# Kernel optimization log

Measured on AMD Instinct MI355X. Metric: run time of the kernel, lower is better.

## Reference

```python
import jax, jax.numpy as jnp
import numpy as np

ALPHA, GAMMA = 0.25, 2.0
MD_THRES = 0.5
BF, AF, VAR = 1.0, 0.5, 1.0  # mining_param chosen to exercise the DAS (dynamic anchor selection) path
BETA = 1.0 / 9.0
EPS = 1e-8


def rbox_corners(boxes):
    # boxes [N,5] = (cx, cy, w, h, angle_deg) -> corners [N,4,2]
    cx, cy, w, h, a = (boxes[:, i] for i in range(5))
    t = a * (jnp.pi / 180.0)
    c, s = jnp.cos(t), jnp.sin(t)
    lx = jnp.array([-0.5, 0.5, 0.5, -0.5], boxes.dtype)
    ly = jnp.array([-0.5, -0.5, 0.5, 0.5], boxes.dtype)
    dx = w[:, None] * lx[None, :]
    dy = h[:, None] * ly[None, :]
    x = cx[:, None] + dx * c[:, None] - dy * s[:, None]
    y = cy[:, None] + dx * s[:, None] + dy * c[:, None]
    return jnp.stack([x, y], axis=-1)


def _pts_in_poly(pts, poly):
    # pts [P,2], poly [4,2] convex quad -> [P] bool
    e = jnp.roll(poly, -1, axis=0) - poly
    rel = pts[:, None, :] - poly[None, :, :]
    cr = e[None, :, 0] * rel[:, :, 1] - e[None, :, 1] * rel[:, :, 0]
    return jnp.all(cr >= -1e-6, axis=1) | jnp.all(cr <= 1e-6, axis=1)


def _pair_inter_area(ca, cb):
    # exact convex quad-quad intersection area; ca, cb: [4,2]
    p, q = ca, cb
    r = jnp.roll(ca, -1, axis=0) - ca
    s = jnp.roll(cb, -1, axis=0) - cb
    rxs = r[:, None, 0] * s[None, :, 1] - r[:, None, 1] * s[None, :, 0]  # [4,4]
    qp = q[None, :, :] - p[:, None, :]
    qpxs = qp[..., 0] * s[None, :, 1] - qp[..., 1] * s[None, :, 0]
    qpxr = qp[..., 0] * r[:, None, 1] - qp[..., 1] * r[:, None, 0]
    denom = jnp.where(jnp.abs(rxs) > 1e-10, rxs, 1.0)
    t = qpxs / denom
    u = qpxr / denom
    valid = (jnp.abs(rxs) > 1e-10) & (t >= 0) & (t <= 1) & (u >= 0) & (u <= 1)
    ipts = p[:, None, :] + t[..., None] * r[:, None, :]  # [4,4,2]
    cand = jnp.concatenate([ca, cb, ipts.reshape(16, 2)], axis=0)  # [24,2]
    mask = jnp.concatenate([_pts_in_poly(ca, cb), _pts_in_poly(cb, ca), valid.reshape(16)])
    n = mask.sum()
    center = (cand * mask[:, None]).sum(0) / jnp.maximum(n, 1)
    d = cand - center
    ang = jnp.where(mask, jnp.arctan2(d[:, 1], d[:, 0]), 1e9)
    order = jnp.argsort(ang)  # valid points first, CCW order
    sp = cand[order]
    sm = mask[order]
    sp = jnp.where(sm[:, None], sp, sp[0])  # pad with first vertex (zero shoelace contribution)
    nx = jnp.roll(sp, -1, axis=0)
    area = 0.5 * jnp.abs(jnp.sum(sp[:, 0] * nx[:, 1] - nx[:, 0] * sp[:, 1]))
    return jnp.where(n >= 3, area, 0.0)


def rbox_iou(boxes_a, boxes_b, indicator, thresh=0.1):
    # exact rotated IoU, computed only where axis-aligned indicator >= thresh (else 0)
    ca = rbox_corners(boxes_a)
    cb = rbox_corners(boxes_b)
    inter = jax.vmap(lambda a: jax.vmap(lambda b: _pair_inter_area(a, b))(cb))(ca)  # [N,M]
    area_a = (boxes_a[:, 2] * boxes_a[:, 3])[:, None]
    area_b = (boxes_b[:, 2] * boxes_b[:, 3])[None, :]
    iou = inter / (area_a + area_b - inter + EPS)
    return jnp.where(indicator >= thresh, iou, 0.0)


def min_area_square(rb):
    s = jnp.maximum(rb[:, 2], rb[:, 3]) * 0.5
    return jnp.stack([rb[:, 0] - s, rb[:, 1] - s, rb[:, 0] + s, rb[:, 1] + s], axis=1)


def bbox_overlaps(a, b):
    # axis-aligned IoU, a [N,4], b [M,4] (xyxy)
    lt = jnp.maximum(a[:, None, :2], b[None, :, :2])
    rb = jnp.minimum(a[:, None, 2:], b[None, :, 2:])
    wh = jnp.clip(rb - lt, 0.0)
    inter = wh[..., 0] * wh[..., 1]
    aa = (a[:, 2] - a[:, 0]) * (a[:, 3] - a[:, 1])
    ab = (b[:, 2] - b[:, 0]) * (b[:, 3] - b[:, 1])
    return inter / (aa[:, None] + ab[None, :] - inter + EPS)


def box_encode(ex, gt):
    gw = jnp.maximum(gt[:, 2], 1.0)
    gh = jnp.maximum(gt[:, 3], 1.0)
    dx = (gt[:, 0] - ex[:, 0]) / ex[:, 2]
    dy = (gt[:, 1] - ex[:, 1]) / ex[:, 3]
    dw = jnp.log(gw / ex[:, 2])
    dh = jnp.log(gh / ex[:, 3])
    dt = jnp.tan(gt[:, 4] * jnp.pi / 180.0) - jnp.tan(ex[:, 4] * jnp.pi / 180.0)
    return jnp.stack([dx, dy, dw, dh, dt], axis=1)


def _image_loss(cls, reg, anc, ranc, ann):
    A, C = cls.shape
    M = ann.shape[0]
    gt = ann[:, :5]
    labels = ann[:, 5].astype(jnp.int32)
    cls = jnp.clip(cls, 1e-4, 1.0 - 1e-4)
    ov_bf = rbox_iou(anc, gt, bbox_overlaps(min_area_square(anc), min_area_square(gt)))
    ov_af = rbox_iou(ranc, gt, bbox_overlaps(min_area_square(ranc), min_area_square(gt)))
    md = jnp.abs(BF * ov_bf + AF * ov_af - jnp.abs(ov_af - ov_bf) ** VAR)
    md = jax.lax.stop_gradient(md)  # original computes overlaps via numpy (no grad)
    iou_max = md.max(1)
    iou_argmax = md.argmax(1)
    pos = iou_max >= MD_THRES
    max_gt = md.max(0)
    argmax_gt = md.argmax(0)
    force = jnp.zeros((A,), jnp.int32).at[argmax_gt].add((max_gt < MD_THRES).astype(jnp.int32)) > 0
    pos = pos | force
    num_pos = pos.sum()
    # DAS matching weights (rows only meaningful at positive anchors; computed full + masked)
    md_p = jnp.where(pos[:, None], md, -jnp.inf)
    max_pos = md_p.max(0)   # [M]
    arg_pos = md_p.argmax(0)
    pos_mask = (md >= MD_THRES) & pos[:, None]
    pos_mask = pos_mask.at[arg_pos, jnp.arange(M)].set(True)
    comp = jnp.where(pos_mask, 1.0 - max_pos[None, :], md)
    mw_max = (comp + md).max(1)  # matching_weight.max(1)[0]
    # classification targets: -1 ignore / 0 neg / 1 pos-class
    assigned = gt[iou_argmax]
    alab = labels[iou_argmax]
    onehot = alab[:, None] == jnp.arange(C)[None, :]
    tgt = jnp.broadcast_to(jnp.where(iou_max < MD_THRES - 0.1, 0.0, -1.0)[:, None], (A, C))
    tgt = jnp.where(pos[:, None], 0.0, tgt)
    tgt = jnp.where(pos[:, None] & onehot, 1.0, tgt)
    af = jnp.where(tgt == 1.0, ALPHA, 1.0 - ALPHA)
    fw = af * jnp.where(tgt == 1.0, 1.0 - cls, cls) ** GAMMA
    bce = -(tgt * jnp.log(cls + 1e-6) + (1.0 - tgt) * jnp.log(1.0 - cls + 1e-6))
    sw = jnp.where(tgt == 0.0, 1.0, 0.0)
    sw = jnp.where(pos[:, None] & onehot, mw_max[:, None] + 1.0, sw)
    cls_loss = jnp.where(tgt != -1.0, fw * bce * sw, 0.0)
    cls_l = cls_loss.sum() / jnp.maximum(num_pos.astype(cls.dtype), 1.0)
    reg_t = box_encode(anc, assigned)
    diff = jnp.abs(reg - reg_t)
    sl1 = jnp.where(diff < BETA, 0.5 * diff ** 2 / BETA, diff - 0.5 * BETA) * mw_max[:, None]
    sl1 = jnp.where(pos[:, None], sl1, 0.0)
    reg_l = jnp.where(num_pos > 0, sl1.sum() / jnp.maximum(num_pos * 5, 1).astype(cls.dtype), 0.0)
    return cls_l, reg_l


def _forward(classifications, regressions, anchors, refined_achors, annotations):
    B = classifications.shape[0]
    cl, rl = [], []
    for j in range(B):  # small fixed batch loop, as in the original
        c, r = _image_loss(classifications[j], regressions[j], anchors[j], refined_achors[j], annotations[j])
        cl.append(c)
        rl.append(r)
    loss_cls = jnp.stack(cl).mean(keepdims=True)
    loss_reg = jnp.stack(rl).mean(keepdims=True)
    return loss_cls, loss_reg


def _rand_boxes(key, shape):
    k1, k2, k3, k4, k5 = jax.random.split(key, 5)
    cx = jax.random.uniform(k1, shape, minval=32.0, maxval=992.0)
    cy = jax.random.uniform(k2, shape, minval=32.0, maxval=992.0)
    w = jax.random.uniform(k3, shape, minval=16.0, maxval=160.0)
    h = jax.random.uniform(k4, shape, minval=16.0, maxval=160.0)
    a = jax.random.uniform(k5, shape, minval=-30.0, maxval=30.0)
    return jnp.stack([cx, cy, w, h, a], axis=-1)


def setup_inputs() -> dict:
    key = jax.random.key(0)
    ks = jax.random.split(key, 6)
    B, A, M, C = 2, 16384, 32, 15
    classifications = jax.random.uniform(ks[0], (B, A, C), minval=0.02, maxval=0.98)
    regressions = 0.1 * jax.random.normal(ks[1], (B, A, 5))
    anchors = _rand_boxes(ks[2], (B, A))
    noise = 0.05 * jax.random.normal(ks[3], (B, A, 5))
    refined_achors = anchors + noise * jnp.array([8.0, 8.0, 4.0, 4.0, 5.0])
    gt = _rand_boxes(ks[4], (B, M))
    labels = jax.random.randint(ks[5], (B, M, 1), 0, C).astype(jnp.float32)
    annotations = jnp.concatenate([gt, labels], axis=-1)  # all labels valid (!= -1)
    return {"classifications": classifications, "regressions": regressions, "anchors": anchors,
            "refined_achors": refined_achors, "annotations": annotations}


def reference(classifications, regressions, anchors, refined_achors, annotations):
    return _forward(classifications, regressions, anchors, refined_achors, annotations)
```

## Files before the change

### kernel.cpp

```cpp
#include <hip/hip_runtime.h>
#include <math.h>

typedef unsigned long long u64;
typedef unsigned int u32;

static constexpr int A = 16384;
static constexpr int M = 32;
static constexpr int C = 15;
static constexpr int B = 2;
static constexpr int NBLK = A / 32;
static constexpr int NBUCKET = 64;
static constexpr int SEGCAP  = 4096;
static constexpr int CAP = NBUCKET * SEGCAP;

static constexpr double PI_D = 3.14159265358979323846;

static constexpr size_t OFF_MD      = 0;
static constexpr size_t OFF_LIST    = OFF_MD + (size_t)B*A*M*4;
static constexpr size_t OFF_PALL    = OFF_LIST + (size_t)CAP*4;
static constexpr size_t OFF_PPOS    = OFF_PALL + (size_t)B*M*NBLK*8;
static constexpr size_t OFF_PCNT    = OFF_PPOS + (size_t)B*M*NBLK*8;
static constexpr size_t OFF_KEYALL  = OFF_PCNT + (size_t)B*NBLK*4;
static constexpr size_t OFF_KEYPOS  = OFF_KEYALL + (size_t)B*M*8;
static constexpr size_t OFF_IOUMAX  = OFF_KEYPOS + (size_t)B*M*8;
static constexpr size_t OFF_IOUARG  = OFF_IOUMAX + (size_t)B*A*4;
static constexpr size_t OFF_POS     = OFF_IOUARG + (size_t)B*A*4;
static constexpr size_t OFF_MAXPOS  = OFF_POS + (size_t)B*A*4;
static constexpr size_t OFF_ARGPOS  = OFF_MAXPOS + (size_t)B*M*4;
static constexpr size_t OFF_NPBASE  = OFF_ARGPOS + (size_t)B*M*4;
static constexpr size_t OFF_NUMPOS  = OFF_NPBASE + (size_t)B*4;
static constexpr size_t OFF_SUMS    = (OFF_NUMPOS + (size_t)B*4 + 7) & ~(size_t)7;
static constexpr size_t OFF_CNTS    = OFF_SUMS + 4*8;
static constexpr size_t CNTS_BYTES  = (size_t)NBUCKET * 32 * 4;

__device__ inline double aa_square_iou(double cx1, double cy1, double s1,
                                       double cx2, double cy2, double s2) {
    double lx = fmax(cx1 - s1, cx2 - s2), ly = fmax(cy1 - s1, cy2 - s2);
    double rx = fmin(cx1 + s1, cx2 + s2), ry = fmin(cy1 + s1, cy2 + s2);
    double w = fmax(rx - lx, 0.0), h = fmax(ry - ly, 0.0);
    double inter = w * h;
    double aa = (2.0 * s1) * (2.0 * s1);
    double ab = (2.0 * s2) * (2.0 * s2);
    return inter / (aa + ab - inter + 1e-8);
}

__device__ inline void rbox_corners1(double cx, double cy, double w, double h,
                                     double adeg, double* X, double* Y) {
    double t = adeg * (PI_D / 180.0);
    double c = cos(t), s = sin(t);
    const double lx[4] = {-0.5, 0.5, 0.5, -0.5};
    const double ly[4] = {-0.5, -0.5, 0.5, 0.5};
#pragma unroll
    for (int i = 0; i < 4; ++i) {
        double dx = w * lx[i], dy = h * ly[i];
        X[i] = cx + dx * c - dy * s;
        Y[i] = cy + dx * s + dy * c;
    }
}

__device__ inline double edges_in_quad_cross_sum(const double* PX, const double* PY,
                                                 const double* QX, const double* QY) {
    double s = 0.0;
#pragma unroll
    for (int k = 0; k < 4; ++k) {
        double x0 = PX[k], y0 = PY[k];
        double x1 = PX[(k + 1) & 3], y1 = PY[(k + 1) & 3];
        double ex = x1 - x0, ey = y1 - y0;
        double t0 = 0.0, t1 = 1.0;
        bool empty = false;
#pragma unroll
        for (int e = 0; e < 4; ++e) {
            double qx0 = QX[e], qy0 = QY[e];
            double qex = QX[(e + 1) & 3] - qx0;
            double qey = QY[(e + 1) & 3] - qy0;
            double d0 = qex * (y0 - qy0) - qey * (x0 - qx0);
            double d1 = qex * (y1 - qy0) - qey * (x1 - qx0);
            if (d0 < 0.0 && d1 < 0.0) empty = true;
            else if (d0 < 0.0) t0 = fmax(t0, d0 / (d0 - d1));
            else if (d1 < 0.0) t1 = fmin(t1, d0 / (d0 - d1));
        }
        if (!empty && t1 > t0) {
            double ax = x0 + t0 * ex, ay = y0 + t0 * ey;
            double bx = x0 + t1 * ex, by = y0 + t1 * ey;
            s += ax * by - ay * bx;
        }
    }
    return s;
}

__device__ inline double quad_inter_area(const double* AX, const double* AY,
                                         const double* BX, const double* BY) {
    double s = edges_in_quad_cross_sum(AX, AY, BX, BY) +
               edges_in_quad_cross_sum(BX, BY, AX, AY);
    return 0.5 * fabs(s);
}

__device__ inline u64 pack_key(float v, u32 inv_idx) {
    return ((u64)__float_as_uint(v) << 32) | (u64)inv_idx;
}

__global__ void k_gate(const float* __restrict__ anc, const float* __restrict__ ranc,
                       const float* __restrict__ ann, float* __restrict__ md,
                       u32* __restrict__ list, u32* __restrict__ cnts,
                       double* __restrict__ sums) {
    __shared__ u32 l_cnt, l_base;
    __shared__ u32 l_idx[256];
    int tid = threadIdx.x;
    if (tid == 0) l_cnt = 0;
    __syncthreads();

    int t = blockIdx.x * 256 + tid;
    if (t < 4) sums[t] = 0.0;
    int m = t & (M - 1);
    int a = (t >> 5) & (A - 1);
    int b = t >> 19;

    const float* pa = anc + ((size_t)(b * A + a)) * 5;
    const float* pr = ranc + ((size_t)(b * A + a)) * 5;
    const float* pg = ann + ((size_t)(b * M + m)) * 6;

    double cxg = pg[0], cyg = pg[1];
    double sg = 0.5 * fmax((double)pg[2], (double)pg[3]);
    double i_bf = aa_square_iou(pa[0], pa[1], 0.5 * fmax((double)pa[2], (double)pa[3]),
                                cxg, cyg, sg);
    double i_af = aa_square_iou(pr[0], pr[1], 0.5 * fmax((double)pr[2], (double)pr[3]),
                                cxg, cyg, sg);
    bool g = (i_bf >= 0.1) || (i_af >= 0.1);
    md[t] = 0.0f;

    if (g) {
        u32 s = atomicAdd(&l_cnt, 1u);
        l_idx[s] = (u32)t;
    }
    __syncthreads();
    u32 n = l_cnt;
    int bucket = blockIdx.x & (NBUCKET - 1);
    if (tid == 0 && n) l_base = atomicAdd(&cnts[bucket * 32], n);
    __syncthreads();
    if ((u32)tid < n) {
        u32 slot = l_base + (u32)tid;
        if (slot < SEGCAP) list[bucket * SEGCAP + slot] = l_idx[tid];
    }
}

__global__ void k_geom(const float* __restrict__ anc, const float* __restrict__ ranc,
                       const float* __restrict__ ann, const u32* __restrict__ list,
                       const u32* __restrict__ cnts, float* __restrict__ md) {
    for (u32 i = blockIdx.x * 256 + threadIdx.x; i < (u32)CAP; i += gridDim.x * 256) {
        u32 bucket = i & (NBUCKET - 1);
        u32 slot = i >> 6;
        if (slot >= cnts[bucket * 32]) continue;
        u32 t = list[bucket * SEGCAP + slot];
        int m = t & (M - 1);
        int a = (t >> 5) & (A - 1);
        int b = t >> 19;
        const float* pa = anc + ((size_t)(b * A + a)) * 5;
        const float* pr = ranc + ((size_t)(b * A + a)) * 5;
        const float* pg = ann + ((size_t)(b * M + m)) * 6;

        double cxg = pg[0], cyg = pg[1], wg = pg[2], hg = pg[3], ag = pg[4];
        double sg = 0.5 * fmax(wg, hg);
        double cxa = pa[0], cya = pa[1], wa = pa[2], ha = pa[3], aa = pa[4];
        double cxr = pr[0], cyr = pr[1], wr = pr[2], hr = pr[3], ar = pr[4];

        double i_bf = aa_square_iou(cxa, cya, 0.5 * fmax(wa, ha), cxg, cyg, sg);
        double i_af = aa_square_iou(cxr, cyr, 0.5 * fmax(wr, hr), cxg, cyg, sg);

        double GX[4], GY[4];
        rbox_corners1(cxg, cyg, wg, hg, ag, GX, GY);
        double areaG = wg * hg;
        double ov_bf = 0.0, ov_af = 0.0;
        if (i_bf >= 0.1) {
            double X[4], Y[4];
            rbox_corners1(cxa, cya, wa, ha, aa, X, Y);
            double inter = quad_inter_area(X, Y, GX, GY);
            ov_bf = inter / (wa * ha + areaG - inter + 1e-8);
        }
        if (i_af >= 0.1) {
            double X[4], Y[4];
            rbox_corners1(cxr, cyr, wr, hr, ar, X, Y);
            double inter = quad_inter_area(X, Y, GX, GY);
            ov_af = inter / (wr * hr + areaG - inter + 1e-8);
        }
        md[t] = (float)fabs(ov_bf + 0.5 * ov_af - fabs(ov_af - ov_bf));
    }
}

__global__ void k_rowcol(const float* __restrict__ md, u64* __restrict__ pAll,
                         u64* __restrict__ pPos, u32* __restrict__ pCnt,
                         float* __restrict__ iou_max, int* __restrict__ iou_arg,
                         int* __restrict__ pos) {
    int blk = blockIdx.x, b = blockIdx.y, tid = threadIdx.x;
    int a0 = blk * 32;
    const float4* src = (const float4*)(md + (size_t)(b * A + a0) * M);
    float4 v4 = src[tid];
    int rr = tid >> 3, c0 = (tid & 7) * 4;
    float vv[4] = {v4.x, v4.y, v4.z, v4.w};

    u64 rowk = 0;
#pragma unroll
    for (int j = 0; j < 4; ++j) {
        u64 k = pack_key(vv[j], 0xFFFFFFFFu - (u32)(c0 + j));
        if (k > rowk) rowk = k;
    }
#pragma unroll
    for (int off = 1; off < 8; off <<= 1) {
        u64 o = __shfl_xor(rowk, off, 8);
        if (o > rowk) rowk = o;
    }
    float rmax = __uint_as_float((u32)(rowk >> 32));
    int p = (rmax >= 0.5f) ? 1 : 0;

    __shared__ u64 lAll[32][32];
    __shared__ u64 lPos[32][32];
    __shared__ int lcnt[32];
    u32 inva = 0xFFFFFFFFu - (u32)(a0 + rr);
#pragma unroll
    for (int j = 0; j < 4; ++j) {
        u64 ck = pack_key(vv[j], inva);
        lAll[rr][c0 + j] = ck;
        lPos[rr][c0 + j] = p ? ck : 0ull;
    }
    if ((tid & 7) == 0) {
        int idx = b * A + a0 + rr;
        iou_max[idx] = rmax;
        iou_arg[idx] = (int)(0xFFFFFFFFu - (u32)(rowk & 0xFFFFFFFFull));
        pos[idx] = p;
        lcnt[rr] = p;
    }
    __syncthreads();
    if (tid < 32) {
        u64 ka = 0, kp = 0;
#pragma unroll
        for (int r = 0; r < 32; ++r) {
            u64 x = lAll[r][tid]; if (x > ka) ka = x;
            u64 y = lPos[r][tid]; if (y > kp) kp = y;
        }
        pAll[((size_t)(b * M + tid)) * NBLK + blk] = ka;
        pPos[((size_t)(b * M + tid)) * NBLK + blk] = kp;
        if (tid == 0) {
            int c = 0;
#pragma unroll
            for (int r = 0; r < 32; ++r) c += lcnt[r];
            pCnt[b * NBLK + blk] = (u32)c;
        }
    }
}

__global__ void k_cols(const u64* __restrict__ pAll, const u64* __restrict__ pPos,
                       const u32* __restrict__ pCnt, u64* __restrict__ keyAll,
                       u64* __restrict__ keyPos, int* __restrict__ npbase) {
    int m = blockIdx.x, b = blockIdx.y, tid = threadIdx.x;
    const u64* pa = pAll + ((size_t)(b * M + m)) * NBLK;
    const u64* pp = pPos + ((size_t)(b * M + m)) * NBLK;
    u64 ka = pa[tid], kp = pp[tid];
    u64 ka2 = pa[tid + 256], kp2 = pp[tid + 256];
    if (ka2 > ka) ka = ka2;
    if (kp2 > kp) kp = kp2;
    __shared__ u64 sa[256], sp[256];
    sa[tid] = ka; sp[tid] = kp;
    __syncthreads();
    for (int s = 128; s > 0; s >>= 1) {
        if (tid < s) {
            if (sa[tid + s] > sa[tid]) sa[tid] = sa[tid + s];
            if (sp[tid + s] > sp[tid]) sp[tid] = sp[tid + s];
        }
        __syncthreads();
    }
    if (tid == 0) {
        keyAll[b * M + m] = sa[0];
        keyPos[b * M + m] = sp[0];
    }
    if (m == 0) {
        __shared__ int sc[256];
        sc[tid] = (int)(pCnt[b * NBLK + tid] + pCnt[b * NBLK + tid + 256]);
        __syncthreads();
        for (int s = 128; s > 0; s >>= 1) {
            if (tid < s) sc[tid] += sc[tid + s];
            __syncthreads();
        }
        if (tid == 0) npbase[b] = sc[0];
    }
}

__global__ void k_fix(const u64* __restrict__ keyAll, const u64* __restrict__ keyPos,
                      const float* __restrict__ md, const int* __restrict__ npbase,
                      int* __restrict__ pos, float* __restrict__ max_pos,
                      int* __restrict__ arg_pos, int* __restrict__ num_pos) {
    int b = blockIdx.x, tid = threadIdx.x;
    __shared__ int s_list[32];
    __shared__ int s_nf, s_new;
    if (tid == 0) { s_nf = 0; s_new = 0; }
    __syncthreads();
    if (tid < 32) {
        u64 k = keyAll[b * M + tid];
        float mx = __uint_as_float((u32)(k >> 32));
        if (mx < 0.5f) {
            int fa = (int)(0xFFFFFFFFu - (u32)(k & 0xFFFFFFFFull));
            int slot = atomicAdd(&s_nf, 1);
            s_list[slot] = fa;
        }
    }
    __syncthreads();
    if (tid < s_nf) {
        int fa = s_list[tid];
        int old = atomicOr(&pos[b * A + fa], 1);
        if (old == 0) atomicAdd(&s_new, 1);
    }
    __syncthreads();
    if (tid < 32) {
        u64 best = keyPos[b * M + tid];
        int nf = s_nf;
        for (int f = 0; f < nf; ++f) {
            int fa = s_list[f];
            float v = md[((size_t)(b * A + fa)) * M + tid];
            u64 k = pack_key(v, 0xFFFFFFFFu - (u32)fa);
            if (k > best) best = k;
        }
        int idx = b * M + tid;
        if (best == 0ull) {
            max_pos[idx] = 0.0f;
            arg_pos[idx] = -1;
        } else {
            max_pos[idx] = __uint_as_float((u32)(best >> 32));
            arg_pos[idx] = (int)(0xFFFFFFFFu - (u32)(best & 0xFFFFFFFFull));
        }
    }
    if (tid == 0) num_pos[b] = npbase[b] + s_new;
}

__global__ void k_loss(const float* __restrict__ cls_in, const float* __restrict__ reg_in,
                       const float* __restrict__ anc, const float* __restrict__ ann,
                       const float* __restrict__ md,
                       const float* __restrict__ iou_max, const int* __restrict__ iou_arg,
                       const int* __restrict__ pos,
                       const float* __restrict__ max_pos, const int* __restrict__ arg_pos,
                       double* __restrict__ sums) {
    int b = blockIdx.y;
    int tid = threadIdx.x;
    int a = blockIdx.x * 256 + tid;

    __shared__ float s_maxpos[M];
    __shared__ int s_argpos[M];
    if (tid < M) {
        s_maxpos[tid] = max_pos[b * M + tid];
        s_argpos[tid] = arg_pos[b * M + tid];
    }
    __syncthreads();

    double csum = 0.0, rsum = 0.0;
    if (a < A) {
        int t = b * A + a;
        float imax = iou_max[t];
        int iarg = iou_arg[t];
        int p = pos[t];

        const float* row = md + (size_t)t * M;
        float mwf = -INFINITY;
#pragma unroll
        for (int m = 0; m < M; ++m) {
            float v = row[m];
            bool pm = (p && v >= 0.5f) || (a == s_argpos[m]);
            float val = pm ? (1.0f - s_maxpos[m] + v) : (v + v);
            mwf = fmaxf(mwf, val);
        }
        double mw = (double)mwf;

        const float* g = ann + ((size_t)(b * M + iarg)) * 6;
        int lab = (int)g[5];
        const float* cp = cls_in + (size_t)t * C;
#pragma unroll
        for (int c = 0; c < C; ++c) {
            double x = (double)cp[c];
            x = fmin(fmax(x, 1e-4), 1.0 - 1e-4);
            double tgt;
            if (p) tgt = (c == lab) ? 1.0 : 0.0;
            else   tgt = (imax < 0.4f) ? 0.0 : -1.0;
            if (tgt >= 0.0) {
                bool one = (tgt == 1.0);
                double af = one ? 0.25 : 0.75;
                double q = one ? (1.0 - x) : x;
                double fw = af * q * q;
                double bce = one ? -log(x + 1e-6) : -log(1.0 - x + 1e-6);
                double sw = one ? (mw + 1.0) : 1.0;
                csum += fw * bce * sw;
            }
        }
        if (p) {
            const float* pa = anc + (size_t)t * 5;
            double gw = fmax((double)g[2], 1.0);
            double gh = fmax((double)g[3], 1.0);
            double rt0 = ((double)g[0] - (double)pa[0]) / (double)pa[2];
            double rt1 = ((double)g[1] - (double)pa[1]) / (double)pa[3];
            double rt2 = log(gw / (double)pa[2]);
            double rt3 = log(gh / (double)pa[3]);
            double rt4 = tan((double)g[4] * (PI_D / 180.0)) - tan((double)pa[4] * (PI_D / 180.0));
            double rt[5] = {rt0, rt1, rt2, rt3, rt4};
            const float* rg = reg_in + (size_t)t * 5;
#pragma unroll
            for (int k = 0; k < 5; ++k) {
                double d = fabs((double)rg[k] - rt[k]);
                double s = (d < (1.0 / 9.0)) ? (0.5 * d * d * 9.0) : (d - 0.5 / 9.0);
                rsum += s * mw;
            }
        }
    }
    __shared__ double scs[256];
    __shared__ double srs[256];
    scs[tid] = csum;
    srs[tid] = rsum;
    __syncthreads();
    for (int s = 128; s > 0; s >>= 1) {
        if (tid < s) { scs[tid] += scs[tid + s]; srs[tid] += srs[tid + s]; }
        __syncthreads();
    }
    if (tid == 0) {
        atomicAdd(&sums[b], scs[0]);
        atomicAdd(&sums[2 + b], srs[0]);
    }
}

__global__ void k_final(const double* __restrict__ sums, const int* __restrict__ num_pos,
                        float* __restrict__ out) {
    if (blockIdx.x == 0 && threadIdx.x == 0) {
        double lc = 0.0, lr = 0.0;
        for (int b = 0; b < B; ++b) {
            double npd = (double)num_pos[b];
            lc += sums[b] / fmax(npd, 1.0);
            int denom = num_pos[b] * 5;
            if (denom < 1) denom = 1;
            lr += (num_pos[b] > 0) ? (sums[2 + b] / (double)denom) : 0.0;
        }
        out[0] = (float)(lc / (double)B);
        out[1] = (float)(lr / (double)B);
    }
}

extern "C" void kernel_launch(void* const* d_in, const int* in_sizes, int n_in,
                              void* d_out, int out_size, void* d_ws, size_t ws_size,
                              hipStream_t stream) {
    const float* cls  = (const float*)d_in[0];
    const float* reg  = (const float*)d_in[1];
    const float* anc  = (const float*)d_in[2];
    const float* ranc = (const float*)d_in[3];
    const float* ann  = (const float*)d_in[4];
    float* out = (float*)d_out;

    char* ws = (char*)d_ws;
    float* md      = (float*)(ws + OFF_MD);
    u32*   list    = (u32*)(ws + OFF_LIST);
    u64*   pAll    = (u64*)(ws + OFF_PALL);
    u64*   pPos    = (u64*)(ws + OFF_PPOS);
    u32*   pCnt    = (u32*)(ws + OFF_PCNT);
    u64*   keyAll  = (u64*)(ws + OFF_KEYALL);
    u64*   keyPos  = (u64*)(ws + OFF_KEYPOS);
    float* iou_max = (float*)(ws + OFF_IOUMAX);
    int*   iou_arg = (int*)(ws + OFF_IOUARG);
    int*   pos     = (int*)(ws + OFF_POS);
    float* max_pos = (float*)(ws + OFF_MAXPOS);
    int*   arg_pos = (int*)(ws + OFF_ARGPOS);
    int*   npbase  = (int*)(ws + OFF_NPBASE);
    int*   num_pos = (int*)(ws + OFF_NUMPOS);
    double* sums   = (double*)(ws + OFF_SUMS);
    u32*   cnts    = (u32*)(ws + OFF_CNTS);

    (void)in_sizes; (void)n_in; (void)out_size; (void)ws_size;

    hipMemsetAsync(cnts, 0, CNTS_BYTES, stream);
    k_gate<<<(B * A * M) / 256, 256, 0, stream>>>(anc, ranc, ann, md, list, cnts, sums);
    k_geom<<<256, 256, 0, stream>>>(anc, ranc, ann, list, cnts, md);
    k_rowcol<<<dim3(NBLK, B), 256, 0, stream>>>(md, pAll, pPos, pCnt,
                                                iou_max, iou_arg, pos);
    k_cols<<<dim3(M, B), 256, 0, stream>>>(pAll, pPos, pCnt, keyAll, keyPos, npbase);
    k_fix<<<B, 64, 0, stream>>>(keyAll, keyPos, md, npbase, pos, max_pos, arg_pos, num_pos);
    k_loss<<<dim3((A + 255) / 256, B), 256, 0, stream>>>(cls, reg, anc, ann, md,
                                                         iou_max, iou_arg, pos,
                                                         max_pos, arg_pos, sums);
    k_final<<<1, 64, 0, stream>>>(sums, num_pos, out);
}
```

Baseline: 111.7 us.

## Fuse column reduction and final loss via last-block pattern, per-block gate lists

```diff
diff --git a/kernel.cpp b/kernel.cpp
--- a/kernel.cpp
+++ b/kernel.cpp
@@ -9,29 +9,26 @@
 static constexpr int C = 15;
 static constexpr int B = 2;
 static constexpr int NBLK = A / 32;
-static constexpr int NBUCKET = 64;
-static constexpr int SEGCAP  = 4096;
-static constexpr int CAP = NBUCKET * SEGCAP;
+static constexpr int NGATE = B * A * M / 256;
+static constexpr int NASSIGN = NBLK * B;
+static constexpr int NLOSS = (A / 256) * B;
 
 static constexpr double PI_D = 3.14159265358979323846;
 
-static constexpr size_t OFF_MD      = 0;
-static constexpr size_t OFF_LIST    = OFF_MD + (size_t)B*A*M*4;
-static constexpr size_t OFF_PALL    = OFF_LIST + (size_t)CAP*4;
-static constexpr size_t OFF_PPOS    = OFF_PALL + (size_t)B*M*NBLK*8;
-static constexpr size_t OFF_PCNT    = OFF_PPOS + (size_t)B*M*NBLK*8;
-static constexpr size_t OFF_KEYALL  = OFF_PCNT + (size_t)B*NBLK*4;
-static constexpr size_t OFF_KEYPOS  = OFF_KEYALL + (size_t)B*M*8;
-static constexpr size_t OFF_IOUMAX  = OFF_KEYPOS + (size_t)B*M*8;
-static constexpr size_t OFF_IOUARG  = OFF_IOUMAX + (size_t)B*A*4;
-static constexpr size_t OFF_POS     = OFF_IOUARG + (size_t)B*A*4;
-static constexpr size_t OFF_MAXPOS  = OFF_POS + (size_t)B*A*4;
-static constexpr size_t OFF_ARGPOS  = OFF_MAXPOS + (size_t)B*M*4;
-static constexpr size_t OFF_NPBASE  = OFF_ARGPOS + (size_t)B*M*4;
-static constexpr size_t OFF_NUMPOS  = OFF_NPBASE + (size_t)B*4;
-static constexpr size_t OFF_SUMS    = (OFF_NUMPOS + (size_t)B*4 + 7) & ~(size_t)7;
-static constexpr size_t OFF_CNTS    = OFF_SUMS + 4*8;
-static constexpr size_t CNTS_BYTES  = (size_t)NBUCKET * 32 * 4;
+static constexpr size_t OFF_MD     = 0;
+static constexpr size_t OFF_LIST   = OFF_MD + (size_t)B*A*M*4;
+static constexpr size_t OFF_SEGC   = OFF_LIST + (size_t)NGATE*256*4;
+static constexpr size_t OFF_PALLT  = OFF_SEGC + (size_t)NGATE*4;
+static constexpr size_t OFF_PPOST  = OFF_PALLT + (size_t)NBLK*64*8;
+static constexpr size_t OFF_PCNT   = OFF_PPOST + (size_t)NBLK*64*8;
+static constexpr size_t OFF_IOUMAX = OFF_PCNT + (size_t)B*NBLK*4;
+static constexpr size_t OFF_IOUARG = OFF_IOUMAX + (size_t)B*A*4;
+static constexpr size_t OFF_POS    = OFF_IOUARG + (size_t)B*A*4;
+static constexpr size_t OFF_MAXPOS = OFF_POS + (size_t)B*A*4;
+static constexpr size_t OFF_ARGPOS = OFF_MAXPOS + (size_t)B*M*4;
+static constexpr size_t OFF_NUMPOS = OFF_ARGPOS + (size_t)B*M*4;
+static constexpr size_t OFF_SUMS   = (OFF_NUMPOS + (size_t)B*4 + 7) & ~(size_t)7;
+static constexpr size_t OFF_DONES  = OFF_SUMS + 4*8;
 
 __device__ inline double aa_square_iou(double cx1, double cy1, double s1,
                                        double cx2, double cy2, double s2) {
@@ -101,9 +98,9 @@
 
 __global__ void k_gate(const float* __restrict__ anc, const float* __restrict__ ranc,
                        const float* __restrict__ ann, float* __restrict__ md,
-                       u32* __restrict__ list, u32* __restrict__ cnts,
-                       double* __restrict__ sums) {
-    __shared__ u32 l_cnt, l_base;
+                       u32* __restrict__ list, u32* __restrict__ segcnt,
+                       double* __restrict__ sums, int* __restrict__ dones) {
+    __shared__ u32 l_cnt;
     __shared__ u32 l_idx[256];
     int tid = threadIdx.x;
     if (tid == 0) l_cnt = 0;
@@ -111,6 +108,7 @@
 
     int t = blockIdx.x * 256 + tid;
     if (t < 4) sums[t] = 0.0;
+    if (t < 2) dones[t] = 0;
     int m = t & (M - 1);
     int a = (t >> 5) & (A - 1);
     int b = t >> 19;
@@ -134,26 +132,22 @@
     }
     __syncthreads();
     u32 n = l_cnt;
-    int bucket = blockIdx.x & (NBUCKET - 1);
-    if (tid == 0 && n) l_base = atomicAdd(&cnts[bucket * 32], n);
-    __syncthreads();
-    if ((u32)tid < n) {
-        u32 slot = l_base + (u32)tid;
-        if (slot < SEGCAP) list[bucket * SEGCAP + slot] = l_idx[tid];
-    }
+    if ((u32)tid < n) list[blockIdx.x * 256 + tid] = l_idx[tid];
+    if (tid == 0) segcnt[blockIdx.x] = n;
 }
 
 __global__ void k_geom(const float* __restrict__ anc, const float* __restrict__ ranc,
                        const float* __restrict__ ann, const u32* __restrict__ list,
-                       const u32* __restrict__ cnts, float* __restrict__ md) {
-    for (u32 i = blockIdx.x * 256 + threadIdx.x; i < (u32)CAP; i += gridDim.x * 256) {
-        u32 bucket = i & (NBUCKET - 1);
-        u32 slot = i >> 6;
-        if (slot >= cnts[bucket * 32]) continue;
-        u32 t = list[bucket * SEGCAP + slot];
+                       const u32* __restrict__ segcnt, float* __restrict__ md) {
+    int gtid = blockIdx.x * 256 + threadIdx.x;
+    int wave = gtid >> 6;
+    int lane = gtid & 63;
+    u32 n = segcnt[wave];
+    for (u32 i = lane; i < n; i += 64) {
+        u32 t = list[wave * 256 + i];
         int m = t & (M - 1);
-        int a = (t >> 5) & (A - 1);
-        int b = t >> 19;
+        int a = ((int)t >> 5) & (A - 1);
+        int b = (int)t >> 19;
         const float* pa = anc + ((size_t)(b * A + a)) * 5;
         const float* pr = ranc + ((size_t)(b * A + a)) * 5;
         const float* pg = ann + ((size_t)(b * M + m)) * 6;
@@ -186,10 +180,12 @@
     }
 }
 
-__global__ void k_rowcol(const float* __restrict__ md, u64* __restrict__ pAll,
-                         u64* __restrict__ pPos, u32* __restrict__ pCnt,
+__global__ void k_assign(const float* __restrict__ md, u64* __restrict__ pAllT,
+                         u64* __restrict__ pPosT, u32* __restrict__ pCnt,
                          float* __restrict__ iou_max, int* __restrict__ iou_arg,
-                         int* __restrict__ pos) {
+                         int* __restrict__ pos, float* __restrict__ max_pos,
+                         int* __restrict__ arg_pos, int* __restrict__ num_pos,
+                         int* __restrict__ dones) {
     int blk = blockIdx.x, b = blockIdx.y, tid = threadIdx.x;
     int a0 = blk * 32;
     const float4* src = (const float4*)(md + (size_t)(b * A + a0) * M);
@@ -236,8 +232,8 @@
             u64 x = lAll[r][tid]; if (x > ka) ka = x;
             u64 y = lPos[r][tid]; if (y > kp) kp = y;
         }
-        pAll[((size_t)(b * M + tid)) * NBLK + blk] = ka;
-        pPos[((size_t)(b * M + tid)) * NBLK + blk] = kp;
+        pAllT[(size_t)blk * 64 + b * 32 + tid] = ka;
+        pPosT[(size_t)blk * 64 + b * 32 + tid] = kp;
         if (tid == 0) {
             int c = 0;
 #pragma unroll
@@ -245,88 +241,77 @@
             pCnt[b * NBLK + blk] = (u32)c;
         }
     }
-}
-
-__global__ void k_cols(const u64* __restrict__ pAll, const u64* __restrict__ pPos,
-                       const u32* __restrict__ pCnt, u64* __restrict__ keyAll,
-                       u64* __restrict__ keyPos, int* __restrict__ npbase) {
-    int m = blockIdx.x, b = blockIdx.y, tid = threadIdx.x;
-    const u64* pa = pAll + ((size_t)(b * M + m)) * NBLK;
-    const u64* pp = pPos + ((size_t)(b * M + m)) * NBLK;
-    u64 ka = pa[tid], kp = pp[tid];
-    u64 ka2 = pa[tid + 256], kp2 = pp[tid + 256];
-    if (ka2 > ka) ka = ka2;
-    if (kp2 > kp) kp = kp2;
-    __shared__ u64 sa[256], sp[256];
-    sa[tid] = ka; sp[tid] = kp;
+
+    __threadfence();
+    __syncthreads();
+    __shared__ int s_last;
+    if (tid == 0) s_last = (atomicAdd(&dones[0], 1) == NASSIGN - 1) ? 1 : 0;
+    __syncthreads();
+    if (!s_last) return;
+    __threadfence();
+
+    int wave = tid >> 6, lane = tid & 63;
+
+    __shared__ int r0[256], r1[256];
+    r0[tid] = (int)(pCnt[tid] + pCnt[tid + 256]);
+    r1[tid] = (int)(pCnt[512 + tid] + pCnt[768 + tid]);
     __syncthreads();
     for (int s = 128; s > 0; s >>= 1) {
-        if (tid < s) {
-            if (sa[tid + s] > sa[tid]) sa[tid] = sa[tid + s];
-            if (sp[tid + s] > sp[tid]) sp[tid] = sp[tid + s];
-        }
+        if (tid < s) { r0[tid] += r0[tid + s]; r1[tid] += r1[tid + s]; }
         __syncthreads();
     }
-    if (tid == 0) {
-        keyAll[b * M + m] = sa[0];
-        keyPos[b * M + m] = sp[0];
-    }
-    if (m == 0) {
-        __shared__ int sc[256];
-        sc[tid] = (int)(pCnt[b * NBLK + tid] + pCnt[b * NBLK + tid + 256]);
-        __syncthreads();
-        for (int s = 128; s > 0; s >>= 1) {
-            if (tid < s) sc[tid] += sc[tid + s];
-            __syncthreads();
-        }
-        if (tid == 0) npbase[b] = sc[0];
-    }
-}
-
-__global__ void k_fix(const u64* __restrict__ keyAll, const u64* __restrict__ keyPos,
-                      const float* __restrict__ md, const int* __restrict__ npbase,
-                      int* __restrict__ pos, float* __restrict__ max_pos,
-                      int* __restrict__ arg_pos, int* __restrict__ num_pos) {
-    int b = blockIdx.x, tid = threadIdx.x;
-    __shared__ int s_list[32];
-    __shared__ int s_nf, s_new;
-    if (tid == 0) { s_nf = 0; s_new = 0; }
-    __syncthreads();
-    if (tid < 32) {
-        u64 k = keyAll[b * M + tid];
-        float mx = __uint_as_float((u32)(k >> 32));
-        if (mx < 0.5f) {
-            int fa = (int)(0xFFFFFFFFu - (u32)(k & 0xFFFFFFFFull));
-            int slot = atomicAdd(&s_nf, 1);
-            s_list[slot] = fa;
-        }
-    }
-    __syncthreads();
-    if (tid < s_nf) {
-        int fa = s_list[tid];
-        int old = atomicOr(&pos[b * A + fa], 1);
-        if (old == 0) atomicAdd(&s_new, 1);
-    }
-    __syncthreads();
-    if (tid < 32) {
-        u64 best = keyPos[b * M + tid];
-        int nf = s_nf;
-        for (int f = 0; f < nf; ++f) {
-            int fa = s_list[f];
-            float v = md[((size_t)(b * A + fa)) * M + tid];
-            u64 k = pack_key(v, 0xFFFFFFFFu - (u32)fa);
-            if (k > best) best = k;
-        }
-        int idx = b * M + tid;
-        if (best == 0ull) {
+    __shared__ int s_npb[2];
+    if (tid == 0) { s_npb[0] = r0[0]; s_npb[1] = r1[0]; }
+
+    u64 ka = 0, kp = 0;
+    for (int t2 = wave * 128; t2 < wave * 128 + 128; ++t2) {
+        u64 x = pAllT[(size_t)t2 * 64 + lane]; if (x > ka) ka = x;
+        u64 y = pPosT[(size_t)t2 * 64 + lane]; if (y > kp) kp = y;
+    }
+    __shared__ u64 redA[256], redP[256];
+    redA[tid] = ka; redP[tid] = kp;
+    __syncthreads();
+
+    __shared__ int s_fl[64];
+    u64 kall = 0, kpos = 0;
+    int fa = -1, newp = 0;
+    int fb = lane >> 5, fm = lane & 31;
+    if (wave == 0) {
+        kall = redA[lane]; kpos = redP[lane];
+#pragma unroll
+        for (int w = 1; w < 4; ++w) {
+            u64 x = redA[w * 64 + lane]; if (x > kall) kall = x;
+            u64 y = redP[w * 64 + lane]; if (y > kpos) kpos = y;
+        }
+        float mxall = __uint_as_float((u32)(kall >> 32));
+        if (mxall < 0.5f) fa = (int)(0xFFFFFFFFu - (u32)(kall & 0xFFFFFFFFull));
+        s_fl[lane] = fa;
+        if (fa >= 0) {
+            int old = atomicOr(&pos[fb * A + fa], 1);
+            newp = (old == 0) ? 1 : 0;
+        }
+    }
+    __syncthreads();
+    if (wave == 0) {
+        for (int f = 0; f < 64; ++f) {
+            int fa2 = s_fl[f];
+            if (fa2 < 0 || (f >> 5) != fb) continue;
+            float v = md[((size_t)(fb * A + fa2)) * M + fm];
+            u64 k = pack_key(v, 0xFFFFFFFFu - (u32)fa2);
+            if (k > kpos) kpos = k;
+        }
+        int idx = fb * M + fm;
+        if (kpos == 0ull) {
             max_pos[idx] = 0.0f;
             arg_pos[idx] = -1;
         } else {
-            max_pos[idx] = __uint_as_float((u32)(best >> 32));
-            arg_pos[idx] = (int)(0xFFFFFFFFu - (u32)(best & 0xFFFFFFFFull));
-        }
-    }
-    if (tid == 0) num_pos[b] = npbase[b] + s_new;
+            max_pos[idx] = __uint_as_float((u32)(kpos >> 32));
+            arg_pos[idx] = (int)(0xFFFFFFFFu - (u32)(kpos & 0xFFFFFFFFull));
+        }
+        u64 ball = __ballot(newp != 0);
+        if (lane == 0) num_pos[0] = s_npb[0] + __popcll(ball & 0xFFFFFFFFull);
+        if (lane == 32) num_pos[1] = s_npb[1] + __popcll(ball >> 32);
+    }
 }
 
 __global__ void k_loss(const float* __restrict__ cls_in, const float* __restrict__ reg_in,
@@ -335,7 +320,9 @@
                        const float* __restrict__ iou_max, const int* __restrict__ iou_arg,
                        const int* __restrict__ pos,
                        const float* __restrict__ max_pos, const int* __restrict__ arg_pos,
-                       double* __restrict__ sums) {
+                       const int* __restrict__ num_pos,
+                       double* __restrict__ sums, int* __restrict__ dones,
+                       float* __restrict__ out) {
     int b = blockIdx.y;
     int tid = threadIdx.x;
     int a = blockIdx.x * 256 + tid;
@@ -349,20 +336,25 @@
     __syncthreads();
 
     double csum = 0.0, rsum = 0.0;
-    if (a < A) {
+    {
         int t = b * A + a;
         float imax = iou_max[t];
         int iarg = iou_arg[t];
         int p = pos[t];
 
-        const float* row = md + (size_t)t * M;
-        float mwf = -INFINITY;
-#pragma unroll
-        for (int m = 0; m < M; ++m) {
-            float v = row[m];
-            bool pm = (p && v >= 0.5f) || (a == s_argpos[m]);
-            float val = pm ? (1.0f - s_maxpos[m] + v) : (v + v);
-            mwf = fmaxf(mwf, val);
+        float mwf;
+        if (p) {
+            const float* row = md + (size_t)t * M;
+            mwf = -INFINITY;
+#pragma unroll
+            for (int m = 0; m < M; ++m) {
+                float v = row[m];
+                bool pm = (v >= 0.5f) || (a == s_argpos[m]);
+                float val = pm ? (1.0f - s_maxpos[m] + v) : (v + v);
+                mwf = fmaxf(mwf, val);
+            }
+        } else {
+            mwf = imax + imax;
         }
         double mw = (double)mwf;
 
@@ -418,18 +410,21 @@
         atomicAdd(&sums[b], scs[0]);
         atomicAdd(&sums[2 + b], srs[0]);
     }
-}
-
-__global__ void k_final(const double* __restrict__ sums, const int* __restrict__ num_pos,
-                        float* __restrict__ out) {
-    if (blockIdx.x == 0 && threadIdx.x == 0) {
+
+    __threadfence();
+    __syncthreads();
+    __shared__ int s_last;
+    if (tid == 0) s_last = (atomicAdd(&dones[1], 1) == NLOSS - 1) ? 1 : 0;
+    __syncthreads();
+    if (s_last && tid == 0) {
+        __threadfence();
         double lc = 0.0, lr = 0.0;
-        for (int b = 0; b < B; ++b) {
-            double npd = (double)num_pos[b];
-            lc += sums[b] / fmax(npd, 1.0);
-            int denom = num_pos[b] * 5;
+        for (int bb = 0; bb < B; ++bb) {
+            double npd = (double)num_pos[bb];
+            lc += sums[bb] / fmax(npd, 1.0);
+            int denom = num_pos[bb] * 5;
             if (denom < 1) denom = 1;
-            lr += (num_pos[b] > 0) ? (sums[2 + b] / (double)denom) : 0.0;
+            lr += (num_pos[bb] > 0) ? (sums[2 + bb] / (double)denom) : 0.0;
         }
         out[0] = (float)(lc / (double)B);
         out[1] = (float)(lr / (double)B);
@@ -449,32 +444,27 @@
     char* ws = (char*)d_ws;
     float* md      = (float*)(ws + OFF_MD);
     u32*   list    = (u32*)(ws + OFF_LIST);
-    u64*   pAll    = (u64*)(ws + OFF_PALL);
-    u64*   pPos    = (u64*)(ws + OFF_PPOS);
+    u32*   segcnt  = (u32*)(ws + OFF_SEGC);
+    u64*   pAllT   = (u64*)(ws + OFF_PALLT);
+    u64*   pPosT   = (u64*)(ws + OFF_PPOST);
     u32*   pCnt    = (u32*)(ws + OFF_PCNT);
-    u64*   keyAll  = (u64*)(ws + OFF_KEYALL);
-    u64*   keyPos  = (u64*)(ws + OFF_KEYPOS);
     float* iou_max = (float*)(ws + OFF_IOUMAX);
     int*   iou_arg = (int*)(ws + OFF_IOUARG);
     int*   pos     = (int*)(ws + OFF_POS);
     float* max_pos = (float*)(ws + OFF_MAXPOS);
     int*   arg_pos = (int*)(ws + OFF_ARGPOS);
-    int*   npbase  = (int*)(ws + OFF_NPBASE);
     int*   num_pos = (int*)(ws + OFF_NUMPOS);
     double* sums   = (double*)(ws + OFF_SUMS);
-    u32*   cnts    = (u32*)(ws + OFF_CNTS);
+    int*   dones   = (int*)(ws + OFF_DONES);
 
     (void)in_sizes; (void)n_in; (void)out_size; (void)ws_size;
 
-    hipMemsetAsync(cnts, 0, CNTS_BYTES, stream);
-    k_gate<<<(B * A * M) / 256, 256, 0, stream>>>(anc, ranc, ann, md, list, cnts, sums);
-    k_geom<<<256, 256, 0, stream>>>(anc, ranc, ann, list, cnts, md);
-    k_rowcol<<<dim3(NBLK, B), 256, 0, stream>>>(md, pAll, pPos, pCnt,
-                                                iou_max, iou_arg, pos);
-    k_cols<<<dim3(M, B), 256, 0, stream>>>(pAll, pPos, pCnt, keyAll, keyPos, npbase);
-    k_fix<<<B, 64, 0, stream>>>(keyAll, keyPos, md, npbase, pos, max_pos, arg_pos, num_pos);
-    k_loss<<<dim3((A + 255) / 256, B), 256, 0, stream>>>(cls, reg, anc, ann, md,
-                                                         iou_max, iou_arg, pos,
-                                                         max_pos, arg_pos, sums);
-    k_final<<<1, 64, 0, stream>>>(sums, num_pos, out);
-}
+    k_gate<<<NGATE, 256, 0, stream>>>(anc, ranc, ann, md, list, segcnt, sums, dones);
+    k_geom<<<NGATE / 4, 256, 0, stream>>>(anc, ranc, ann, list, segcnt, md);
+    k_assign<<<dim3(NBLK, B), 256, 0, stream>>>(md, pAllT, pPosT, pCnt, iou_max,
+                                                iou_arg, pos, max_pos, arg_pos,
+                                                num_pos, dones);
+    k_loss<<<dim3(A / 256, B), 256, 0, stream>>>(cls, reg, anc, ann, md, iou_max,
+                                                 iou_arg, pos, max_pos, arg_pos,
+                                                 num_pos, sums, dones, out);
+}
```

New measurement: 226.2 us. 2.03x slower.
